# Performance work log

Hardware: AMD Instinct MI355X
Metric: run time of the kernel (lower is better)

The kernel has to match this reference:

```python
import jax, jax.numpy as jnp
import numpy as np

NUM_HEADS = 8

def dwconv(x, w, b, pad):
    # depthwise conv: x [B, C, H, W], w [C, 1, k, k], groups=C
    y = jax.lax.conv_general_dilated(
        x, w, window_strides=(1, 1), padding=[(pad, pad), (pad, pad)],
        feature_group_count=x.shape[1], dimension_numbers=('NCHW', 'OIHW', 'NCHW'))
    return y + b[None, :, None, None]


def setup_inputs() -> dict:
    key = jax.random.key(0)
    ks = jax.random.split(key, 12)
    B, H, W = 32, 28, 28
    C = 512
    N = 1 + H * W
    Ch = C // NUM_HEADS  # 64
    s = lambda k, shp, fan: jax.random.normal(k, shp, jnp.float32) * (fan ** -0.5)
    return {
        'x': jax.random.normal(ks[0], (B, N, C), jnp.float32),
        'qkv_w': s(ks[1], (3 * C, C), C),
        'qkv_b': jnp.zeros((3 * C,), jnp.float32),
        'proj_w': s(ks[2], (C, C), C),
        'proj_b': jnp.zeros((C,), jnp.float32),
        'w3': s(ks[3], (2 * Ch, 1, 3, 3), 9),
        'b3': jnp.zeros((2 * Ch,), jnp.float32),
        'w5': s(ks[4], (3 * Ch, 1, 5, 5), 25),
        'b5': jnp.zeros((3 * Ch,), jnp.float32),
        'w7': s(ks[5], (3 * Ch, 1, 7, 7), 49),
        'b7': jnp.zeros((3 * Ch,), jnp.float32),
        'H': H,
        'W': W,
    }


def reference(x, qkv_w, qkv_b, proj_w, proj_b, w3, b3, w5, b5, w7, b7, H, W):
    B, N, C = x.shape
    h = NUM_HEADS
    Ch = C // h
    scale = Ch ** -0.5
    # qkv projection -> q, k, v each [B, h, N, Ch]
    qkv = (x @ qkv_w.T + qkv_b).reshape(B, N, 3, h, Ch).transpose(2, 0, 3, 1, 4)
    q, k, v = qkv[0], qkv[1], qkv[2]
    # factorized attention: softmax over tokens on k, then (k^T v) then q @ ...
    k_sm = jax.nn.softmax(k, axis=2)
    kv = jnp.einsum('bhnc,bhnd->bhcd', k_sm, v)          # [B,h,Ch,Ch]
    factor_att = jnp.einsum('bhnc,bhcd->bhnd', q, kv)    # [B,h,N,Ch]
    # conv relative position encoding (CRPE) on image tokens only
    q_img = q[:, :, 1:, :]                               # [B,h,HW,Ch]
    v_img = v[:, :, 1:, :].transpose(0, 1, 3, 2).reshape(B, h * Ch, H, W)
    splits = np.cumsum([2 * Ch, 3 * Ch, 3 * Ch])[:-1]
    v1, v2, v3 = jnp.split(v_img, splits, axis=1)
    conv_v = jnp.concatenate(
        [dwconv(v1, w3, b3, 1), dwconv(v2, w5, b5, 2), dwconv(v3, w7, b7, 3)], axis=1)
    conv_v = conv_v.reshape(B, h, Ch, H * W).transpose(0, 1, 3, 2)  # [B,h,HW,Ch]
    EV = q_img * conv_v
    crpe = jnp.pad(EV, ((0, 0), (0, 0), (1, 0), (0, 0)))  # zero row for cls token
    out = scale * factor_att + crpe
    out = out.transpose(0, 2, 1, 3).reshape(B, N, C)
    return out @ proj_w.T + proj_b
```

## Files before the change

### kernel.cpp

```cpp
#include <hip/hip_runtime.h>
#include <cstdint>
#include <cstddef>


typedef unsigned short u16;

#define HEADS 8
#define CHD   64
#define CDIM  512
#define NTOK  785
#define BATCH 32
#define MROWS (BATCH * NTOK)
#define MPAD  25344
#define QKVN  1536
#define IMGHW 784
#define KVSPLIT 7

typedef float  f32x4  __attribute__((ext_vector_type(4)));
typedef __bf16 bf16x8 __attribute__((ext_vector_type(8)));

__device__ __forceinline__ u16 f2bf(float f) {
  union { float f; uint32_t u; } x; x.f = f;
  uint32_t r = x.u + 0x7fffu + ((x.u >> 16) & 1u);
  return (u16)(r >> 16);
}
__device__ __forceinline__ float bf2f(u16 u) {
  union { uint32_t u; float f; } x; x.u = ((uint32_t)u) << 16;
  return x.f;
}
__device__ __forceinline__ float bflo(uint32_t u) { return bf2f((u16)(u & 0xffffu)); }
__device__ __forceinline__ float bfhi(uint32_t u) { return bf2f((u16)(u >> 16)); }
__device__ __forceinline__ uint32_t pk2(float a, float b) {
#if __has_builtin(__builtin_amdgcn_cvt_pk_bf16_f32)
  auto v = __builtin_amdgcn_cvt_pk_bf16_f32(a, b);
  union { decltype(v) v2; uint32_t u; } cv; cv.v2 = v; return cv.u;
#else
  return (uint32_t)f2bf(a) | ((uint32_t)f2bf(b) << 16);
#endif
}

__global__ __launch_bounds__(256)
void casts_kernel(const float* __restrict__ x, u16* __restrict__ xb,
                  const float* __restrict__ w1, u16* __restrict__ w1b,
                  const float* __restrict__ w2, u16* __restrict__ w2b) {
  const int N1 = MROWS * CDIM / 4, N2 = QKVN * CDIM / 4, N3 = CDIM * CDIM / 4;
  int i = blockIdx.x * 256 + threadIdx.x;
  const float* src; u16* dst;
  if (i < N1)           { src = x;  dst = xb;  }
  else if (i < N1 + N2) { i -= N1;  src = w1; dst = w1b; }
  else if (i < N1 + N2 + N3) { i -= N1 + N2; src = w2; dst = w2b; }
  else return;
  float4 v = reinterpret_cast<const float4*>(src)[i];
  uint2 o; o.x = pk2(v.x, v.y); o.y = pk2(v.z, v.w);
  reinterpret_cast<uint2*>(dst)[i] = o;
}

__device__ __forceinline__ void gld_lds16(const u16* g, u16* l) {
  __builtin_amdgcn_global_load_lds((__attribute__((address_space(1))) void*)g,
                                   (__attribute__((address_space(3))) void*)l,
                                   16, 0, 0);
}

template <int OUTBF16>
__global__ __launch_bounds__(512)
void gemm_bt(const u16* __restrict__ A, const u16* __restrict__ W,
             const float* __restrict__ bias, void* __restrict__ Cout,
             int Mstore, int N, int K, int nMt, int nNt) {
  __shared__ __align__(16) u16 lsA[2][256 * 32];
  __shared__ __align__(16) u16 lsB[2][128 * 32];
  const int flat = blockIdx.x;
  const int xcd = flat & 7, idx = flat >> 3;
  const int nt = idx % nNt;
  const int mt = (idx / nNt) * 8 + xcd;
  if (mt >= nMt) return;
  const int tile_m = mt * 256, tile_n = nt * 128;

  const int tid  = threadIdx.x;
  const int wave = tid >> 6, lane = tid & 63;
  const int quad = lane >> 4, l16 = lane & 15;
  const int wm = (wave & 3) * 64, wn = (wave >> 2) * 64;

  const int srow = tid >> 2;
  const int scol = ((tid & 3) ^ ((tid >> 3) & 3)) * 8;
  const int ldst = tid * 8;

  auto stage = [&](int kt, int buf) {
    const int kc = kt * 32 + scol;
#pragma unroll
    for (int s = 0; s < 2; ++s)
      gld_lds16(A + (size_t)(tile_m + s * 128 + srow) * K + kc,
                &lsA[buf][s * 4096 + ldst]);
    gld_lds16(W + (size_t)(tile_n + srow) * K + kc, &lsB[buf][ldst]);
  };

  f32x4 acc[4][4] = {};

  stage(0, 0);
  __syncthreads();

  const int KT = K >> 5;
  const int pch = (quad ^ ((l16 >> 1) & 3)) * 8;
#pragma unroll 2
  for (int t = 0; t < KT; ++t) {
    const int cur = t & 1;
    if (t + 1 < KT) stage(t + 1, cur ^ 1);
    bf16x8 af[4], bfr[4];
#pragma unroll
    for (int i = 0; i < 4; ++i) {
      af[i]  = *reinterpret_cast<const bf16x8*>(
          &lsA[cur][(wm + i * 16 + l16) * 32 + pch]);
      bfr[i] = *reinterpret_cast<const bf16x8*>(
          &lsB[cur][(wn + i * 16 + l16) * 32 + pch]);
    }
#pragma unroll
    for (int i = 0; i < 4; ++i)
#pragma unroll
      for (int j = 0; j < 4; ++j)
        acc[i][j] = __builtin_amdgcn_mfma_f32_16x16x32_bf16(
            af[i], bfr[j], acc[i][j], 0, 0, 0);
    __syncthreads();
  }

#pragma unroll
  for (int i = 0; i < 4; ++i) {
    const int mbase = tile_m + wm + i * 16 + quad * 4;
#pragma unroll
    for (int j = 0; j < 4; ++j) {
      const int n  = tile_n + wn + j * 16 + l16;
      const float bv = bias[n];
      const float v0 = acc[i][j][0] + bv, v1 = acc[i][j][1] + bv;
      const float v2 = acc[i][j][2] + bv, v3 = acc[i][j][3] + bv;
      if (OUTBF16) {
        u16* cp = reinterpret_cast<u16*>(Cout) + (size_t)mbase * N + n;
        const uint32_t p01 = pk2(v0, v1), p23 = pk2(v2, v3);
        if (mbase + 0 < Mstore) cp[0]            = (u16)p01;
        if (mbase + 1 < Mstore) cp[(size_t)N]    = (u16)(p01 >> 16);
        if (mbase + 2 < Mstore) cp[(size_t)N*2]  = (u16)p23;
        if (mbase + 3 < Mstore) cp[(size_t)N*3]  = (u16)(p23 >> 16);
      } else {
        float* cp = reinterpret_cast<float*>(Cout) + (size_t)mbase * N + n;
        if (mbase + 0 < Mstore) cp[0]           = v0;
        if (mbase + 1 < Mstore) cp[(size_t)N]   = v1;
        if (mbase + 2 < Mstore) cp[(size_t)N*2] = v2;
        if (mbase + 3 < Mstore) cp[(size_t)N*3] = v3;
      }
    }
  }
}

__device__ __forceinline__ void kv_part(
    const u16* __restrict__ qkv, float* __restrict__ kvpart,
    float* __restrict__ kvsum, int bh, int split,
    float* __restrict__ e_s, float* __restrict__ v_s) {
  const int b = bh >> 3, h = bh & 7;
  const int n_start = split * 113;
  const int n_end = min(NTOK, n_start + 113);
  const int t = threadIdx.x;
  const int c4 = (t & 15) * 4;
  const int d4 = (t >> 4) * 4;
  const u16* kbase = qkv + (size_t)(b * NTOK) * QKVN + CDIM + h * CHD;
  const u16* vbase = kbase + CDIM;
  f32x4 acc[4] = {};
  f32x4 sp4 = {0.f, 0.f, 0.f, 0.f};

  for (int n0 = n_start; n0 < n_end; n0 += 32) {
    const int nc = min(32, n_end - n0);
    __syncthreads();
    for (int i4 = t; i4 < nc * 16; i4 += 256) {
      const int nl = i4 >> 4;
      const uint2 kk = *reinterpret_cast<const uint2*>(
          &kbase[(size_t)(n0 + nl) * QKVN + c4]);
      const uint2 vv = *reinterpret_cast<const uint2*>(
          &vbase[(size_t)(n0 + nl) * QKVN + c4]);
      f32x4 e4, v4;
      e4[0] = __expf(bflo(kk.x)); e4[1] = __expf(bfhi(kk.x));
      e4[2] = __expf(bflo(kk.y)); e4[3] = __expf(bfhi(kk.y));
      v4[0] = bflo(vv.x); v4[1] = bfhi(vv.x);
      v4[2] = bflo(vv.y); v4[3] = bfhi(vv.y);
      *reinterpret_cast<f32x4*>(&e_s[nl * 64 + c4]) = e4;
      *reinterpret_cast<f32x4*>(&v_s[nl * 64 + c4]) = v4;
      sp4 += e4;
    }
    __syncthreads();
    for (int nl = 0; nl < nc; ++nl) {
      const f32x4 e4 = *reinterpret_cast<const f32x4*>(&e_s[nl * 64 + c4]);
      const f32x4 v4 = *reinterpret_cast<const f32x4*>(&v_s[nl * 64 + d4]);
      acc[0] += e4[0] * v4;
      acc[1] += e4[1] * v4;
      acc[2] += e4[2] * v4;
      acc[3] += e4[3] * v4;
    }
  }
  float* kb = kvpart + (((size_t)bh * KVSPLIT + split) * 64 + c4) * 64 + d4;
#pragma unroll
  for (int ci = 0; ci < 4; ++ci)
    *reinterpret_cast<f32x4*>(&kb[ci * 64]) = acc[ci];
  __syncthreads();
  *reinterpret_cast<f32x4*>(&e_s[t * 4]) = sp4;
  __syncthreads();
  if (t < 64) {
    float S = 0.f;
#pragma unroll
    for (int m = 0; m < 16; ++m)
      S += e_s[((t >> 2) + 16 * m) * 4 + (t & 3)];
    kvsum[((size_t)bh * KVSPLIT + split) * 64 + t] = S;
  }
}

__global__ __launch_bounds__(256)
void kv_reduce_kernel(const float* __restrict__ kvpart, const float* __restrict__ kvsum,
                      u16* __restrict__ kvT) {
  const int bh = blockIdx.x;
  const int t = threadIdx.x;
  const int d = t & 63, cq = t >> 6;
#pragma unroll
  for (int cc = 0; cc < 16; ++cc) {
    const int c = cq * 16 + cc;
    float s = 0.f, S = 0.f;
#pragma unroll
    for (int sp = 0; sp < KVSPLIT; ++sp) {
      s += kvpart[(((size_t)bh * KVSPLIT + sp) * 64 + c) * 64 + d];
      S += kvsum[((size_t)bh * KVSPLIT + sp) * 64 + c];
    }
    kvT[(size_t)bh * 4096 + d * 64 + c] = f2bf(s / S);
  }
}

template <int KS>
__device__ __forceinline__ void conv_head(
    const u16* __restrict__ qkv, const float* __restrict__ wgt,
    const float* __restrict__ bias, int b, int head, int hh, int yt,
    u16* __restrict__ evbuf, u16* __restrict__ ls, float* __restrict__ wls) {
  constexpr int PAD = KS / 2;
  constexpr int RIN = 4 + 2 * PAD;
  const int t = threadIdx.x;
  const int y0 = yt * 4;
  const u16* vimg = qkv + (size_t)(b * NTOK + 1) * QKVN + 2 * CDIM + head * 64;
  for (int i = t; i < 64 * KS * KS; i += 256)
    wls[i] = wgt[hh * 64 * KS * KS + i];
  const int c8 = (t & 7) * 8;
  for (int pi = t >> 3; pi < RIN * 28; pi += 32) {
    const int ry = pi / 28, rx = pi - ry * 28;
    const int yy = y0 - PAD + ry;
    uint4 val = {0, 0, 0, 0};
    if (yy >= 0 && yy < 28)
      val = *reinterpret_cast<const uint4*>(vimg + (size_t)(yy * 28 + rx) * QKVN + c8);
    *reinterpret_cast<uint4*>(ls + pi * 64 + c8) = val;
  }
  __syncthreads();
  const int d = t & 63, yl = t >> 6;
  float wr[KS * KS];
#pragma unroll
  for (int i = 0; i < KS * KS; ++i) wr[i] = wls[d * KS * KS + i];
  const float bv = bias[hh * 64 + d];
  float acc[28];
#pragma unroll
  for (int x = 0; x < 28; ++x) acc[x] = bv;
#pragma unroll
  for (int xx = 0; xx < 28; ++xx) {
    float col[KS];
#pragma unroll
    for (int r = 0; r < KS; ++r)
      col[r] = bf2f(ls[((yl + r) * 28 + xx) * 64 + d]);
#pragma unroll
    for (int j = 0; j < KS; ++j) {
      const int x = xx + PAD - j;
      if (x >= 0 && x < 28) {
#pragma unroll
        for (int r = 0; r < KS; ++r)
          acc[x] += col[r] * wr[r * KS + j];
      }
    }
  }
  const int p0 = (y0 + yl) * 28;
  const u16* qrow = qkv + (size_t)(b * NTOK + 1 + p0) * QKVN + head * 64 + d;
  u16* obase = evbuf + (((size_t)(b * 8 + head)) * IMGHW + p0) * 64 + d;
#pragma unroll
  for (int x = 0; x < 28; ++x) {
    const float ev = acc[x] * bf2f(qrow[(size_t)x * QKVN]);
    obase[(size_t)x * 64] = f2bf(ev);
  }
}

__global__ __launch_bounds__(256)
void kv_conv_kernel(const u16* __restrict__ qkv, float* __restrict__ kvpart,
                    float* __restrict__ kvsum,
                    const float* __restrict__ w3, const float* __restrict__ b3,
                    const float* __restrict__ w5, const float* __restrict__ b5,
                    const float* __restrict__ w7, const float* __restrict__ b7,
                    u16* __restrict__ evbuf) {
  __shared__ __align__(16) char smem[10 * 28 * 64 * 2 + 64 * 49 * 4];
  const int y = blockIdx.y;
  if (y < KVSPLIT) {
    float* e_s = reinterpret_cast<float*>(smem);
    float* v_s = e_s + 32 * 64;
    kv_part(qkv, kvpart, kvsum, blockIdx.x, y, e_s, v_s);
  } else {
    u16* ls = reinterpret_cast<u16*>(smem);
    float* wls = reinterpret_cast<float*>(smem + 10 * 28 * 64 * 2);
    const int b = blockIdx.x >> 3, h = blockIdx.x & 7, yt = y - KVSPLIT;
    if (h < 2)      conv_head<3>(qkv, w3, b3, b, h, h,     yt, evbuf, ls, wls);
    else if (h < 5) conv_head<5>(qkv, w5, b5, b, h, h - 2, yt, evbuf, ls, wls);
    else            conv_head<7>(qkv, w7, b7, b, h, h - 5, yt, evbuf, ls, wls);
  }
}

__global__ __launch_bounds__(256)
void combine_kernel(const u16* __restrict__ qkv, const u16* __restrict__ kvT,
                    const u16* __restrict__ evbuf, u16* __restrict__ attn) {
  __shared__ __align__(16) float sa[128 * 64];
  const int bh = blockIdx.x;
  const int b = bh >> 3, h = bh & 7;
  const int t = threadIdx.x;
  const int wave = t >> 6, lane = t & 63;
  const int quad = lane >> 4, l16 = lane & 15;
  const int tokbase = blockIdx.y * 256 + wave * 64;

  const u16* kvb = kvT + (size_t)bh * 4096;
  bf16x8 bfr[4][2];
#pragma unroll
  for (int j = 0; j < 4; ++j)
#pragma unroll
    for (int kk = 0; kk < 2; ++kk)
      bfr[j][kk] = *reinterpret_cast<const bf16x8*>(
          &kvb[(j * 16 + l16) * 64 + kk * 32 + quad * 8]);

  bf16x8 af[4][2];
#pragma unroll
  for (int i = 0; i < 4; ++i) {
    const int tok = min(tokbase + i * 16 + l16, NTOK - 1);
    const u16* qrow = qkv + (size_t)(b * NTOK + tok) * QKVN + h * CHD;
    af[i][0] = *reinterpret_cast<const bf16x8*>(&qrow[quad * 8]);
    af[i][1] = *reinterpret_cast<const bf16x8*>(&qrow[32 + quad * 8]);
  }

  f32x4 acc[4][4] = {};
#pragma unroll
  for (int kk = 0; kk < 2; ++kk)
#pragma unroll
    for (int i = 0; i < 4; ++i)
#pragma unroll
      for (int j = 0; j < 4; ++j)
        acc[i][j] = __builtin_amdgcn_mfma_f32_16x16x32_bf16(af[i][kk], bfr[j][kk], acc[i][j], 0, 0, 0);

  const float scale = 0.125f;
  const u16* evb = evbuf + (size_t)bh * IMGHW * 64;
#pragma unroll
  for (int half = 0; half < 2; ++half) {
    if ((wave >> 1) == half) {
      const int rbase = (wave & 1) * 64;
#pragma unroll
      for (int i = 0; i < 4; ++i)
#pragma unroll
        for (int rr = 0; rr < 4; ++rr) {
          const int rl = rbase + i * 16 + quad * 4 + rr;
#pragma unroll
          for (int j = 0; j < 4; ++j) {
            const int dd = j * 16 + l16;
            sa[rl * 64 + (((dd >> 2) ^ (rl & 15)) * 4) + (dd & 3)] =
                scale * acc[i][j][rr];
          }
        }
    }
    __syncthreads();
    {
      const int rl = t >> 1;
      const int tok = blockIdx.y * 256 + half * 128 + rl;
      if (tok < NTOK) {
        u16* orow = attn + (size_t)(b * NTOK + tok) * CDIM + h * CHD;
        const int cb = (t & 1) * 8;
#pragma unroll
        for (int c2 = 0; c2 < 4; ++c2) {
          const int ch0 = cb + c2 * 2;
          const f32x4 v0 = *reinterpret_cast<const f32x4*>(
              &sa[rl * 64 + ((ch0 ^ (rl & 15)) * 4)]);
          const f32x4 v1 = *reinterpret_cast<const f32x4*>(
              &sa[rl * 64 + (((ch0 + 1) ^ (rl & 15)) * 4)]);
          float o0 = v0[0], o1 = v0[1], o2 = v0[2], o3 = v0[3];
          float o4 = v1[0], o5 = v1[1], o6 = v1[2], o7 = v1[3];
          if (tok > 0) {
            const uint4 ev = *reinterpret_cast<const uint4*>(
                &evb[(size_t)(tok - 1) * 64 + ch0 * 4]);
            o0 += bflo(ev.x); o1 += bfhi(ev.x);
            o2 += bflo(ev.y); o3 += bfhi(ev.y);
            o4 += bflo(ev.z); o5 += bfhi(ev.z);
            o6 += bflo(ev.w); o7 += bfhi(ev.w);
          }
          uint4 ow;
          ow.x = pk2(o0, o1); ow.y = pk2(o2, o3);
          ow.z = pk2(o4, o5); ow.w = pk2(o6, o7);
          *reinterpret_cast<uint4*>(&orow[ch0 * 4]) = ow;
        }
      }
    }
    __syncthreads();
  }
}

extern "C" void kernel_launch(void* const* d_in, const int* in_sizes, int n_in,
                              void* d_out, int out_size, void* d_ws, size_t ws_size,
                              hipStream_t stream) {
  const float* x      = (const float*)d_in[0];
  const float* qkv_w  = (const float*)d_in[1];
  const float* qkv_b  = (const float*)d_in[2];
  const float* proj_w = (const float*)d_in[3];
  const float* proj_b = (const float*)d_in[4];
  const float* w3 = (const float*)d_in[5];
  const float* b3 = (const float*)d_in[6];
  const float* w5 = (const float*)d_in[7];
  const float* b5 = (const float*)d_in[8];
  const float* w7 = (const float*)d_in[9];
  const float* b7 = (const float*)d_in[10];
  float* out = (float*)d_out;

  char* p = (char*)d_ws;
  u16* xb    = (u16*)p;   p += (size_t)MPAD * CDIM * 2;
  u16* wqb   = (u16*)p;   p += (size_t)QKVN * CDIM * 2;
  u16* wpb   = (u16*)p;   p += (size_t)CDIM * CDIM * 2;
  u16* qkvb  = (u16*)p;   p += (size_t)MPAD * QKVN * 2;
  float* kvsum = (float*)p; p += (size_t)256 * KVSPLIT * 64 * 4;
  u16* kvT   = (u16*)p;   p += (size_t)256 * 64 * 64 * 2;
  float* kvpart = (float*)p; p += (size_t)256 * KVSPLIT * 64 * 64 * 4;
  u16* attn  = (u16*)p;   p += (size_t)MPAD * CDIM * 2;
  u16* evbuf = xb;

  {
    const int total = MROWS * CDIM / 4 + QKVN * CDIM / 4 + CDIM * CDIM / 4;
    casts_kernel<<<(total + 255) / 256, 256, 0, stream>>>(x, xb, qkv_w, wqb, proj_w, wpb);
  }
  gemm_bt<1><<<13 * 8 * 12, 512, 0, stream>>>(xb, wqb, qkv_b, qkvb,
                                              MPAD, QKVN, CDIM, 99, 12);
  kv_conv_kernel<<<dim3(256, KVSPLIT + 7), 256, 0, stream>>>(
      qkvb, kvpart, kvsum, w3, b3, w5, b5, w7, b7, evbuf);
  kv_reduce_kernel<<<256, 256, 0, stream>>>(kvpart, kvsum, kvT);
  combine_kernel<<<dim3(256, 4), 256, 0, stream>>>(qkvb, kvT, evbuf, attn);
  gemm_bt<0><<<13 * 8 * 4, 512, 0, stream>>>(attn, wpb, proj_b, out,
                                             MROWS, CDIM, CDIM, 99, 4);
}
```

Before: 305.4 us.

## Compute full-token KV per block and drop split-reduce kernel

Removes the 7-way token split of the softmax(K)^T V computation. Each (batch, head) block now loops over all 785 tokens, normalizes by the column sums itself, and writes bf16 kvT directly. This eliminates the partial-sum buffers, their global round trip and the separate reduce kernel launch. The cost is fewer blocks doing the KV work (256 instead of 1792), each with a 7x longer serial loop, so those blocks may become the tail of the fused kv/conv grid.

After: 295.2 us. 1.03x faster.

```diff
diff --git a/kernel.cpp b/kernel.cpp
--- a/kernel.cpp
+++ b/kernel.cpp
@@ -14,7 +14,6 @@
 #define MPAD  25344
 #define QKVN  1536
 #define IMGHW 784
-#define KVSPLIT 7
 
 typedef float  f32x4  __attribute__((ext_vector_type(4)));
 typedef __bf16 bf16x8 __attribute__((ext_vector_type(8)));
@@ -149,12 +148,9 @@
 }
 
 __device__ __forceinline__ void kv_part(
-    const u16* __restrict__ qkv, float* __restrict__ kvpart,
-    float* __restrict__ kvsum, int bh, int split,
+    const u16* __restrict__ qkv, u16* __restrict__ kvT, int bh,
     float* __restrict__ e_s, float* __restrict__ v_s) {
   const int b = bh >> 3, h = bh & 7;
-  const int n_start = split * 113;
-  const int n_end = min(NTOK, n_start + 113);
   const int t = threadIdx.x;
   const int c4 = (t & 15) * 4;
   const int d4 = (t >> 4) * 4;
@@ -163,8 +159,8 @@
   f32x4 acc[4] = {};
   f32x4 sp4 = {0.f, 0.f, 0.f, 0.f};
 
-  for (int n0 = n_start; n0 < n_end; n0 += 32) {
-    const int nc = min(32, n_end - n0);
+  for (int n0 = 0; n0 < NTOK; n0 += 32) {
+    const int nc = min(32, NTOK - n0);
     __syncthreads();
     for (int i4 = t; i4 < nc * 16; i4 += 256) {
       const int nl = i4 >> 4;
@@ -191,10 +187,6 @@
       acc[3] += e4[3] * v4;
     }
   }
-  float* kb = kvpart + (((size_t)bh * KVSPLIT + split) * 64 + c4) * 64 + d4;
-#pragma unroll
-  for (int ci = 0; ci < 4; ++ci)
-    *reinterpret_cast<f32x4*>(&kb[ci * 64]) = acc[ci];
   __syncthreads();
   *reinterpret_cast<f32x4*>(&e_s[t * 4]) = sp4;
   __syncthreads();
@@ -203,26 +195,17 @@
 #pragma unroll
     for (int m = 0; m < 16; ++m)
       S += e_s[((t >> 2) + 16 * m) * 4 + (t & 3)];
-    kvsum[((size_t)bh * KVSPLIT + split) * 64 + t] = S;
-  }
-}
-
-__global__ __launch_bounds__(256)
-void kv_reduce_kernel(const float* __restrict__ kvpart, const float* __restrict__ kvsum,
-                      u16* __restrict__ kvT) {
-  const int bh = blockIdx.x;
-  const int t = threadIdx.x;
-  const int d = t & 63, cq = t >> 6;
-#pragma unroll
-  for (int cc = 0; cc < 16; ++cc) {
-    const int c = cq * 16 + cc;
-    float s = 0.f, S = 0.f;
-#pragma unroll
-    for (int sp = 0; sp < KVSPLIT; ++sp) {
-      s += kvpart[(((size_t)bh * KVSPLIT + sp) * 64 + c) * 64 + d];
-      S += kvsum[((size_t)bh * KVSPLIT + sp) * 64 + c];
-    }
-    kvT[(size_t)bh * 4096 + d * 64 + c] = f2bf(s / S);
+    v_s[t] = S;
+  }
+  __syncthreads();
+  const float S0 = v_s[c4], S1 = v_s[c4 + 1], S2 = v_s[c4 + 2], S3 = v_s[c4 + 3];
+  u16* kb = kvT + (size_t)bh * 4096 + (size_t)d4 * 64 + c4;
+#pragma unroll
+  for (int di = 0; di < 4; ++di) {
+    uint2 o;
+    o.x = pk2(acc[0][di] / S0, acc[1][di] / S1);
+    o.y = pk2(acc[2][di] / S2, acc[3][di] / S3);
+    *reinterpret_cast<uint2*>(&kb[(size_t)di * 64]) = o;
   }
 }
 
@@ -283,22 +266,21 @@
 }
 
 __global__ __launch_bounds__(256)
-void kv_conv_kernel(const u16* __restrict__ qkv, float* __restrict__ kvpart,
-                    float* __restrict__ kvsum,
+void kv_conv_kernel(const u16* __restrict__ qkv, u16* __restrict__ kvT,
                     const float* __restrict__ w3, const float* __restrict__ b3,
                     const float* __restrict__ w5, const float* __restrict__ b5,
                     const float* __restrict__ w7, const float* __restrict__ b7,
                     u16* __restrict__ evbuf) {
   __shared__ __align__(16) char smem[10 * 28 * 64 * 2 + 64 * 49 * 4];
   const int y = blockIdx.y;
-  if (y < KVSPLIT) {
+  if (y == 0) {
     float* e_s = reinterpret_cast<float*>(smem);
     float* v_s = e_s + 32 * 64;
-    kv_part(qkv, kvpart, kvsum, blockIdx.x, y, e_s, v_s);
+    kv_part(qkv, kvT, blockIdx.x, e_s, v_s);
   } else {
     u16* ls = reinterpret_cast<u16*>(smem);
     float* wls = reinterpret_cast<float*>(smem + 10 * 28 * 64 * 2);
-    const int b = blockIdx.x >> 3, h = blockIdx.x & 7, yt = y - KVSPLIT;
+    const int b = blockIdx.x >> 3, h = blockIdx.x & 7, yt = y - 1;
     if (h < 2)      conv_head<3>(qkv, w3, b3, b, h, h,     yt, evbuf, ls, wls);
     else if (h < 5) conv_head<5>(qkv, w5, b5, b, h, h - 2, yt, evbuf, ls, wls);
     else            conv_head<7>(qkv, w7, b7, b, h, h - 5, yt, evbuf, ls, wls);
@@ -418,9 +400,7 @@
   u16* wqb   = (u16*)p;   p += (size_t)QKVN * CDIM * 2;
   u16* wpb   = (u16*)p;   p += (size_t)CDIM * CDIM * 2;
   u16* qkvb  = (u16*)p;   p += (size_t)MPAD * QKVN * 2;
-  float* kvsum = (float*)p; p += (size_t)256 * KVSPLIT * 64 * 4;
   u16* kvT   = (u16*)p;   p += (size_t)256 * 64 * 64 * 2;
-  float* kvpart = (float*)p; p += (size_t)256 * KVSPLIT * 64 * 64 * 4;
   u16* attn  = (u16*)p;   p += (size_t)MPAD * CDIM * 2;
   u16* evbuf = xb;
 
@@ -430,9 +410,8 @@
   }
   gemm_bt<1><<<13 * 8 * 12, 512, 0, stream>>>(xb, wqb, qkv_b, qkvb,
                                               MPAD, QKVN, CDIM, 99, 12);
-  kv_conv_kernel<<<dim3(256, KVSPLIT + 7), 256, 0, stream>>>(
-      qkvb, kvpart, kvsum, w3, b3, w5, b5, w7, b7, evbuf);
-  kv_reduce_kernel<<<256, 256, 0, stream>>>(kvpart, kvsum, kvT);
+  kv_conv_kernel<<<dim3(256, 8), 256, 0, stream>>>(
+      qkvb, kvT, w3, b3, w5, b5, w7, b7, evbuf);
   combine_kernel<<<dim3(256, 4), 256, 0, stream>>>(qkvb, kvT, evbuf, attn);
   gemm_bt<0><<<13 * 8 * 4, 512, 0, stream>>>(attn, wpb, proj_b, out,
                                              MROWS, CDIM, CDIM, 99, 4);
```
